# Kernel optimization log

Measured on AMD Instinct MI355X. Metric: run time of the kernel, lower is better.

The kernel has to match this reference:

```python
import jax, jax.numpy as jnp
import numpy as np

HEADS = 12
DIM_HEAD = 64
SCALE = DIM_HEAD ** -0.5

def setup_inputs() -> dict:
    key = jax.random.key(0)
    k1, k2, k3, k4 = jax.random.split(key, 4)
    dim, inner = 768, HEADS * DIM_HEAD
    x = jax.random.normal(k1, (4, 2048, dim), dtype=jnp.float32)
    w_qkv = jax.random.normal(k2, (dim, 3 * inner), dtype=jnp.float32) * (dim ** -0.5)
    w_out = jax.random.normal(k3, (inner, dim), dtype=jnp.float32) * (inner ** -0.5)
    b_out = jax.random.normal(k4, (dim,), dtype=jnp.float32) * 0.02
    return {"x": x, "w_qkv": w_qkv, "w_out": w_out, "b_out": b_out}

def reference(x, w_qkv, w_out, b_out):
    B, N, _ = x.shape
    qkv = jnp.einsum('bnd,de->bne', x, w_qkv)  # [B,N,3*inner]
    q, k, v = jnp.split(qkv, 3, axis=-1)
    # b n (h d) -> b h n d
    split_heads = lambda t: t.reshape(B, N, HEADS, DIM_HEAD).transpose(0, 2, 1, 3)
    q, k, v = split_heads(q), split_heads(k), split_heads(v)
    dots = jnp.einsum('bhnd,bhmd->bhnm', q, k) * SCALE  # [B,H,N,N]
    attn = jax.nn.softmax(dots, axis=-1)
    out = jnp.einsum('bhnm,bhmd->bhnd', attn, v)
    out = out.transpose(0, 2, 1, 3).reshape(B, N, HEADS * DIM_HEAD)  # b h n d -> b n (h d)
    return jnp.einsum('bne,ed->bnd', out, w_out) + b_out
```

## Files before the change

kernel.cpp:

```cpp
#include <hip/hip_runtime.h>
#include <stdint.h>

typedef unsigned short ushort_t;
typedef __attribute__((ext_vector_type(8))) short short8;
typedef __attribute__((ext_vector_type(4))) float f32x4;
typedef __attribute__((ext_vector_type(2))) uint32_t u32x2;

#define BATCH 4
#define SEQ 2048
#define DMODEL 768
#define NH 12
#define HD 64
#define QKV3 2304
#define NHEADS 48
#define SCALE_Q 0.18033688011112042f

__device__ __forceinline__ ushort_t f2bf(float f) {
    union { float f; uint32_t u; } v; v.f = f;
    uint32_t u = v.u;
    u += 0x7FFF + ((u >> 16) & 1);
    return (ushort_t)(u >> 16);
}

__device__ __forceinline__ uint32_t pack_bf16(float a, float b) {
#if __has_builtin(__builtin_amdgcn_cvt_pk_bf16_f32)
    typedef __attribute__((ext_vector_type(2))) __bf16 bf16x2;
    bf16x2 r = __builtin_amdgcn_cvt_pk_bf16_f32(a, b);
    return __builtin_bit_cast(uint32_t, r);
#else
    return ((uint32_t)f2bf(b) << 16) | (uint32_t)f2bf(a);
#endif
}

typedef __attribute__((address_space(1))) uint32_t as1_u32;
typedef __attribute__((address_space(3))) uint32_t as3_u32;
__device__ __forceinline__ void async16(void* lds, const void* gsrc) {
    __builtin_amdgcn_global_load_lds((as1_u32*)gsrc, (as3_u32*)lds, 16, 0, 0);
}

__device__ __forceinline__ void wait_vm_lgkm0() {
    __builtin_amdgcn_s_waitcnt(0x0070);
}

__device__ __forceinline__ void swap32(uint32_t& a, uint32_t& b) {
    asm("v_permlane32_swap_b32 %0, %1" : "+v"(a), "+v"(b));
}
__device__ __forceinline__ void swap16(uint32_t& a, uint32_t& b) {
    asm("v_permlane16_swap_b32 %0, %1" : "+v"(a), "+v"(b));
}

__global__ __launch_bounds__(256) void cvt_bf16(
    const float* __restrict__ in, ushort_t* __restrict__ out) {
    int i = blockIdx.x * 256 + threadIdx.x;
    float4 v = *(const float4*)(in + (size_t)i * 4);
    ushort4 o; o.x = f2bf(v.x); o.y = f2bf(v.y); o.z = f2bf(v.z); o.w = f2bf(v.w);
    *(ushort4*)(out + (size_t)i * 4) = o;
}

__global__ __launch_bounds__(256) void transpose_f32_bf16(
    const float* __restrict__ in, ushort_t* __restrict__ out, int R, int C) {
    __shared__ ushort_t t[64][72];
    const int tid = threadIdx.x;
    const int r0 = blockIdx.y * 64, c0 = blockIdx.x * 64;
#pragma unroll
    for (int i = 0; i < 4; i++) {
        int idx = tid + i * 256;
        int row = idx >> 4, c4 = (idx & 15) * 4;
        float4 v = *(const float4*)(in + (size_t)(r0 + row) * C + c0 + c4);
        ushort4 o; o.x = f2bf(v.x); o.y = f2bf(v.y); o.z = f2bf(v.z); o.w = f2bf(v.w);
        *(ushort4*)&t[row][c4] = o;
    }
    __syncthreads();
#pragma unroll
    for (int i = 0; i < 2; i++) {
        int idx = tid + i * 256;
        int oc = idx >> 3, g8 = (idx & 7) * 8;
        ushort_t tmp[8];
#pragma unroll
        for (int e = 0; e < 8; e++) tmp[e] = t[g8 + e][oc];
        *(short8*)(out + (size_t)(c0 + oc) * R + r0 + g8) = *(const short8*)tmp;
    }
}

__global__ __launch_bounds__(256, 2) void gemm_qkv(
    const ushort_t* __restrict__ A, const ushort_t* __restrict__ B,
    ushort_t* __restrict__ qkv, ushort_t* __restrict__ vT) {
    __shared__ ushort_t As[128 * 64];
    __shared__ ushort_t Bs[128 * 64];

    const int tid = threadIdx.x;
    const int m0 = blockIdx.y * 128, n0 = blockIdx.x * 128;
    const int lane = tid & 63, w = tid >> 6;
    const int wm = w >> 1, wn = w & 1;
    const int l16 = lane & 15, quad = lane >> 4;

    f32x4 acc[4][4];
#pragma unroll
    for (int i = 0; i < 4; i++)
#pragma unroll
        for (int j = 0; j < 4; j++) acc[i][j] = (f32x4){0.f, 0.f, 0.f, 0.f};

    int srow[4], scol[4];
#pragma unroll
    for (int j = 0; j < 4; j++) {
        int s = j * 256 + tid;
        srow[j] = s >> 3;
        scol[j] = ((s & 7) ^ (srow[j] & 7)) * 8;
    }
    const int swz0 = (quad ^ (l16 & 7)) * 8;
    const int swz1 = ((4 + quad) ^ (l16 & 7)) * 8;

    for (int kt = 0; kt < DMODEL; kt += 64) {
#pragma unroll
        for (int j = 0; j < 4; j++) {
            async16(&As[(j * 256 + w * 64) * 8],
                    A + (size_t)(m0 + srow[j]) * DMODEL + kt + scol[j]);
            async16(&Bs[(j * 256 + w * 64) * 8],
                    B + (size_t)(n0 + srow[j]) * DMODEL + kt + scol[j]);
        }
        wait_vm_lgkm0();
        __syncthreads();

        short8 a[4][2], b[4][2];
#pragma unroll
        for (int mi = 0; mi < 4; mi++) {
            int r = (wm * 64 + mi * 16 + l16) * 64;
            a[mi][0] = *(const short8*)&As[r + swz0];
            a[mi][1] = *(const short8*)&As[r + swz1];
        }
#pragma unroll
        for (int ni = 0; ni < 4; ni++) {
            int r = (wn * 64 + ni * 16 + l16) * 64;
            b[ni][0] = *(const short8*)&Bs[r + swz0];
            b[ni][1] = *(const short8*)&Bs[r + swz1];
        }
#pragma unroll
        for (int kk = 0; kk < 2; kk++)
#pragma unroll
            for (int mi = 0; mi < 4; mi++)
#pragma unroll
                for (int ni = 0; ni < 4; ni++)
                    acc[mi][ni] = __builtin_amdgcn_mfma_f32_16x16x32_bf16(
                        a[mi][kk], b[ni][kk], acc[mi][ni], 0, 0, 0);
        __syncthreads();
    }

#pragma unroll
    for (int ni = 0; ni < 4; ni++) {
        int nbase = n0 + wn * 64 + ni * 16;
        int which = nbase / DMODEL;
        int rem = nbase - which * DMODEL;
        int h = rem >> 6;
        int d = (rem & 63) + l16;
        if (which == 2) {
#pragma unroll
            for (int mi = 0; mi < 4; mi++) {
                int mg = m0 + wm * 64 + mi * 16 + quad * 4;
                int b_ = mg >> 11, ns = mg & 2047;
                u32x2 pk = {pack_bf16(acc[mi][ni][0], acc[mi][ni][1]),
                            pack_bf16(acc[mi][ni][2], acc[mi][ni][3])};
                *(u32x2*)(vT + ((size_t)(b_ * NH + h) * HD + d) * SEQ + ns) = pk;
            }
        } else {
            float scale = (which == 0) ? SCALE_Q : 1.0f;
#pragma unroll
            for (int mi = 0; mi < 4; mi++) {
#pragma unroll
                for (int r = 0; r < 4; r++) {
                    int mg = m0 + wm * 64 + mi * 16 + quad * 4 + r;
                    int b_ = mg >> 11, ns = mg & 2047;
                    size_t dst = (((size_t)(which * BATCH + b_) * NH + h) * SEQ + ns) * HD + d;
                    qkv[dst] = f2bf(acc[mi][ni][r] * scale);
                }
            }
        }
    }
}

__global__ __launch_bounds__(256, 3) void attn(
    const ushort_t* __restrict__ qkv, const ushort_t* __restrict__ vT,
    ushort_t* __restrict__ ao) {
    __shared__ ushort_t smem[16384];

    const int tid = threadIdx.x;
    const int bid = blockIdx.x;
    const int i = bid >> 3;
    const int bh = (bid & 7) + 8 * (i % 6);
    const int qt = i / 6;
    const int lane = tid & 63, w = tid >> 6;
    const int l16 = lane & 15, quad = lane >> 4;
    const int qh7 = l16 & 7;

    const ushort_t* qh = qkv + (size_t)bh * (SEQ * HD);
    const ushort_t* kh = qkv + (size_t)(NHEADS + bh) * (SEQ * HD);
    const ushort_t* vh = vT + (size_t)bh * (HD * SEQ);

    short8 aq[2][2];
#pragma unroll
    for (int mi = 0; mi < 2; mi++)
#pragma unroll
        for (int kk = 0; kk < 2; kk++) {
            int row = qt * 128 + w * 32 + mi * 16 + l16;
            aq[mi][kk] = *(const short8*)(qh + (size_t)row * HD + kk * 32 + quad * 8);
        }

    short8 ones8;
#pragma unroll
    for (int j = 0; j < 8; j++) ones8[j] = (short)0x3F80;

    f32x4 acc_l[2];
    f32x4 O[4][2];
#pragma unroll
    for (int mi = 0; mi < 2; mi++) acc_l[mi] = (f32x4){0.f, 0.f, 0.f, 0.f};
#pragma unroll
    for (int nd = 0; nd < 4; nd++)
#pragma unroll
        for (int mi = 0; mi < 2; mi++) O[nd][mi] = (f32x4){0.f, 0.f, 0.f, 0.f};

    int srow[2], scol[2];
#pragma unroll
    for (int j = 0; j < 2; j++) {
        int s = j * 256 + tid;
        srow[j] = s >> 3;
        scol[j] = ((s & 7) ^ (srow[j] & 7)) * 8;
    }
    const int swz0 = (quad ^ qh7) * 8;
    const int swz1 = ((4 + quad) ^ qh7) * 8;

#pragma unroll
    for (int j = 0; j < 2; j++) {
        async16(&smem[(j * 256 + w * 64) * 8],
                kh + (size_t)srow[j] * HD + scol[j]);
        async16(&smem[4096 + (j * 256 + w * 64) * 8],
                vh + (size_t)srow[j] * SEQ + scol[j]);
    }

    const int NT = SEQ / 64;
    for (int t = 0; t < NT; t++) {
        wait_vm_lgkm0();
        __syncthreads();
        if (t + 1 < NT) {
            int nb = ((t + 1) & 1) * 8192, j1 = (t + 1) * 64;
#pragma unroll
            for (int j = 0; j < 2; j++) {
                async16(&smem[nb + (j * 256 + w * 64) * 8],
                        kh + (size_t)(j1 + srow[j]) * HD + scol[j]);
                async16(&smem[nb + 4096 + (j * 256 + w * 64) * 8],
                        vh + (size_t)srow[j] * SEQ + j1 + scol[j]);
            }
        }
        const ushort_t* Ks = smem + (t & 1) * 8192;
        const ushort_t* Vs = Ks + 4096;

#pragma unroll
        for (int p = 0; p < 2; p++) {
            uint32_t pkv[2][2][2];
#pragma unroll
            for (int sub = 0; sub < 2; sub++) {
                const int ni = p * 2 + sub;
                int r = (ni * 16 + l16) * 64;
                short8 ak0 = *(const short8*)&Ks[r + swz0];
                short8 ak1 = *(const short8*)&Ks[r + swz1];
#pragma unroll
                for (int mi = 0; mi < 2; mi++) {
                    f32x4 s = __builtin_amdgcn_mfma_f32_16x16x32_bf16(
                        ak0, aq[mi][0], (f32x4){0.f, 0.f, 0.f, 0.f}, 0, 0, 0);
                    s = __builtin_amdgcn_mfma_f32_16x16x32_bf16(
                        ak1, aq[mi][1], s, 0, 0, 0);
                    f32x4 pr;
#pragma unroll
                    for (int rr = 0; rr < 4; rr++)
                        pr[rr] = __builtin_amdgcn_exp2f(s[rr]);
                    pkv[sub][mi][0] = pack_bf16(pr[0], pr[1]);
                    pkv[sub][mi][1] = pack_bf16(pr[2], pr[3]);
                }
            }
            short8 bp32[2];
#pragma unroll
            for (int mi = 0; mi < 2; mi++) {
                uint32_t x0 = pkv[0][mi][0], y0 = pkv[1][mi][0];
                uint32_t x1 = pkv[0][mi][1], y1 = pkv[1][mi][1];
                swap32(x0, y0); swap16(x0, y0);
                swap32(x1, y1); swap16(x1, y1);
                union { short8 s; uint32_t u[4]; } bu;
                bu.u[0] = x0; bu.u[1] = x1; bu.u[2] = y0; bu.u[3] = y1;
                bp32[mi] = bu.s;
            }
            __builtin_amdgcn_s_setprio(1);
#pragma unroll
            for (int mi = 0; mi < 2; mi++)
                acc_l[mi] = __builtin_amdgcn_mfma_f32_16x16x32_bf16(
                    ones8, bp32[mi], acc_l[mi], 0, 0, 0);
#pragma unroll
            for (int nd = 0; nd < 4; nd++) {
                int vrow = nd * 16 + l16;
                short8 av = *(const short8*)&Vs[vrow * 64 +
                                                (((p * 4 + quad) ^ qh7) * 8)];
#pragma unroll
                for (int mi = 0; mi < 2; mi++)
                    O[nd][mi] = __builtin_amdgcn_mfma_f32_16x16x32_bf16(
                        av, bp32[mi], O[nd][mi], 0, 0, 0);
            }
            __builtin_amdgcn_s_setprio(0);
        }
    }

    float inv[2];
#pragma unroll
    for (int mi = 0; mi < 2; mi++)
        inv[mi] = __builtin_amdgcn_rcpf(acc_l[mi][0]);
    wait_vm_lgkm0();
    __syncthreads();
    ushort_t* Lt = smem;
#pragma unroll
    for (int mi = 0; mi < 2; mi++)
#pragma unroll
        for (int nd = 0; nd < 4; nd++) {
            int row = w * 32 + mi * 16 + l16;
            int col = nd * 16 + quad * 4;
            uint32_t d0 = pack_bf16(O[nd][mi][0] * inv[mi], O[nd][mi][1] * inv[mi]);
            uint32_t d1 = pack_bf16(O[nd][mi][2] * inv[mi], O[nd][mi][3] * inv[mi]);
            *(u32x2*)&Lt[row * 72 + col] = (u32x2){d0, d1};
        }
    __syncthreads();

    const int b_ = bh / NH, h = bh % NH;
#pragma unroll
    for (int i2 = 0; i2 < 4; i2++) {
        int idx = tid + i2 * 256;
        int row = idx >> 3, c8 = (idx & 7) * 8;
        short8 vv = *(const short8*)&Lt[row * 72 + c8];
        *(short8*)(ao + ((size_t)(b_ * SEQ + qt * 128 + row)) * DMODEL +
                   h * HD + c8) = vv;
    }
}

__global__ __launch_bounds__(256, 2) void gemm_out(
    const ushort_t* __restrict__ A, const ushort_t* __restrict__ B,
    const float* __restrict__ bias, float* __restrict__ out) {
    __shared__ ushort_t As[128 * 64];
    __shared__ ushort_t Bs[128 * 64];

    const int tid = threadIdx.x;
    const int m0 = blockIdx.y * 128, n0 = blockIdx.x * 128;
    const int lane = tid & 63, w = tid >> 6;
    const int wm = w >> 1, wn = w & 1;
    const int l16 = lane & 15, quad = lane >> 4;

    f32x4 acc[4][4];
#pragma unroll
    for (int i = 0; i < 4; i++)
#pragma unroll
        for (int j = 0; j < 4; j++) acc[i][j] = (f32x4){0.f, 0.f, 0.f, 0.f};

    int srow[4], scol[4];
#pragma unroll
    for (int j = 0; j < 4; j++) {
        int s = j * 256 + tid;
        srow[j] = s >> 3;
        scol[j] = ((s & 7) ^ (srow[j] & 7)) * 8;
    }
    const int swz0 = (quad ^ (l16 & 7)) * 8;
    const int swz1 = ((4 + quad) ^ (l16 & 7)) * 8;

    for (int kt = 0; kt < DMODEL; kt += 64) {
#pragma unroll
        for (int j = 0; j < 4; j++) {
            async16(&As[(j * 256 + w * 64) * 8],
                    A + (size_t)(m0 + srow[j]) * DMODEL + kt + scol[j]);
            async16(&Bs[(j * 256 + w * 64) * 8],
                    B + (size_t)(n0 + srow[j]) * DMODEL + kt + scol[j]);
        }
        wait_vm_lgkm0();
        __syncthreads();

        short8 a[4][2], b[4][2];
#pragma unroll
        for (int mi = 0; mi < 4; mi++) {
            int r = (wm * 64 + mi * 16 + l16) * 64;
            a[mi][0] = *(const short8*)&As[r + swz0];
            a[mi][1] = *(const short8*)&As[r + swz1];
        }
#pragma unroll
        for (int ni = 0; ni < 4; ni++) {
            int r = (wn * 64 + ni * 16 + l16) * 64;
            b[ni][0] = *(const short8*)&Bs[r + swz0];
            b[ni][1] = *(const short8*)&Bs[r + swz1];
        }
#pragma unroll
        for (int kk = 0; kk < 2; kk++)
#pragma unroll
            for (int mi = 0; mi < 4; mi++)
#pragma unroll
                for (int ni = 0; ni < 4; ni++)
                    acc[mi][ni] = __builtin_amdgcn_mfma_f32_16x16x32_bf16(
                        a[mi][kk], b[ni][kk], acc[mi][ni], 0, 0, 0);
        __syncthreads();
    }

#pragma unroll
    for (int ni = 0; ni < 4; ni++) {
        int ng = n0 + wn * 64 + ni * 16 + l16;
        float bv = bias[ng];
#pragma unroll
        for (int mi = 0; mi < 4; mi++) {
#pragma unroll
            for (int r = 0; r < 4; r++) {
                int mg = m0 + wm * 64 + mi * 16 + quad * 4 + r;
                out[(size_t)mg * DMODEL + ng] = acc[mi][ni][r] + bv;
            }
        }
    }
}

extern "C" void kernel_launch(void* const* d_in, const int* in_sizes, int n_in,
                              void* d_out, int out_size, void* d_ws, size_t ws_size,
                              hipStream_t stream) {
    const float* x     = (const float*)d_in[0];
    const float* w_qkv = (const float*)d_in[1];
    const float* w_out = (const float*)d_in[2];
    const float* b_out = (const float*)d_in[3];
    float* out = (float*)d_out;

    ushort_t* xb  = (ushort_t*)d_ws;
    ushort_t* wqT = xb  + (size_t)8192 * 768;
    ushort_t* woT = wqT + (size_t)QKV3 * 768;
    ushort_t* qkv = woT + (size_t)768 * 768;
    ushort_t* vT  = qkv + (size_t)3 * NHEADS * SEQ * HD;
    ushort_t* ao  = vT  + (size_t)NHEADS * HD * SEQ;

    cvt_bf16<<<dim3((8192 * 768) / 4 / 256), 256, 0, stream>>>(x, xb);
    transpose_f32_bf16<<<dim3(QKV3 / 64, DMODEL / 64), 256, 0, stream>>>(
        w_qkv, wqT, DMODEL, QKV3);
    transpose_f32_bf16<<<dim3(DMODEL / 64, DMODEL / 64), 256, 0, stream>>>(
        w_out, woT, DMODEL, DMODEL);

    gemm_qkv<<<dim3(QKV3 / 128, (BATCH * SEQ) / 128), 256, 0, stream>>>(
        xb, wqT, qkv, vT);

    attn<<<dim3(NHEADS * (SEQ / 128)), 256, 0, stream>>>(qkv, vT, ao);

    gemm_out<<<dim3(DMODEL / 128, (BATCH * SEQ) / 128), 256, 0, stream>>>(
        ao, woT, b_out, out);
}
```

Measured before the change: 211.1 us.

## Load V tiles directly into registers instead of staging through LDS

V fragments are now loaded from global memory straight into registers, double-buffered across a two-tile unrolled loop, instead of being copied asynchronously into shared memory and read back. This halves the LDS footprint and removes the LDS reads for V. Each wave now issues its own redundant global loads of V, since all four waves read the same tile, and register pressure rises by 16 short8 values, which may hurt occupancy under launch_bounds 3.

```diff
diff --git a/kernel.cpp b/kernel.cpp
--- a/kernel.cpp
+++ b/kernel.cpp
@@ -180,7 +180,7 @@
 __global__ __launch_bounds__(256, 3) void attn(
     const ushort_t* __restrict__ qkv, const ushort_t* __restrict__ vT,
     ushort_t* __restrict__ ao) {
-    __shared__ ushort_t smem[16384];
+    __shared__ ushort_t smem[9216];
 
     const int tid = threadIdx.x;
     const int bid = blockIdx.x;
@@ -194,6 +194,7 @@
     const ushort_t* qh = qkv + (size_t)bh * (SEQ * HD);
     const ushort_t* kh = qkv + (size_t)(NHEADS + bh) * (SEQ * HD);
     const ushort_t* vh = vT + (size_t)bh * (HD * SEQ);
+    const ushort_t* vbase = vh + (size_t)l16 * SEQ + quad * 8;
 
     short8 aq[2][2];
 #pragma unroll
@@ -227,30 +228,35 @@
     const int swz0 = (quad ^ qh7) * 8;
     const int swz1 = ((4 + quad) ^ qh7) * 8;
 
-#pragma unroll
-    for (int j = 0; j < 2; j++) {
+    auto vload = [&](short8 (&vd)[8], int t) {
+#pragma unroll
+        for (int p = 0; p < 2; p++)
+#pragma unroll
+            for (int nd = 0; nd < 4; nd++)
+                vd[p * 4 + nd] = *(const short8*)(
+                    vbase + (size_t)nd * 16 * SEQ + t * 64 + p * 32);
+    };
+
+#pragma unroll
+    for (int j = 0; j < 2; j++)
         async16(&smem[(j * 256 + w * 64) * 8],
                 kh + (size_t)srow[j] * HD + scol[j]);
-        async16(&smem[4096 + (j * 256 + w * 64) * 8],
-                vh + (size_t)srow[j] * SEQ + scol[j]);
-    }
+    short8 vA[8], vB[8];
+    vload(vA, 0);
 
     const int NT = SEQ / 64;
-    for (int t = 0; t < NT; t++) {
+    auto tile_body = [&](short8 (&vcur)[8], short8 (&vnxt)[8], int t) {
         wait_vm_lgkm0();
         __syncthreads();
         if (t + 1 < NT) {
-            int nb = ((t + 1) & 1) * 8192, j1 = (t + 1) * 64;
-#pragma unroll
-            for (int j = 0; j < 2; j++) {
+            int nb = ((t + 1) & 1) * 4096, j1 = (t + 1) * 64;
+#pragma unroll
+            for (int j = 0; j < 2; j++)
                 async16(&smem[nb + (j * 256 + w * 64) * 8],
                         kh + (size_t)(j1 + srow[j]) * HD + scol[j]);
-                async16(&smem[nb + 4096 + (j * 256 + w * 64) * 8],
-                        vh + (size_t)srow[j] * SEQ + j1 + scol[j]);
-            }
-        }
-        const ushort_t* Ks = smem + (t & 1) * 8192;
-        const ushort_t* Vs = Ks + 4096;
+            vload(vnxt, t + 1);
+        }
+        const ushort_t* Ks = smem + (t & 1) * 4096;
 
 #pragma unroll
         for (int p = 0; p < 2; p++) {
@@ -293,16 +299,18 @@
                     ones8, bp32[mi], acc_l[mi], 0, 0, 0);
 #pragma unroll
             for (int nd = 0; nd < 4; nd++) {
-                int vrow = nd * 16 + l16;
-                short8 av = *(const short8*)&Vs[vrow * 64 +
-                                                (((p * 4 + quad) ^ qh7) * 8)];
 #pragma unroll
                 for (int mi = 0; mi < 2; mi++)
                     O[nd][mi] = __builtin_amdgcn_mfma_f32_16x16x32_bf16(
-                        av, bp32[mi], O[nd][mi], 0, 0, 0);
+                        vcur[p * 4 + nd], bp32[mi], O[nd][mi], 0, 0, 0);
             }
             __builtin_amdgcn_s_setprio(0);
         }
+    };
+
+    for (int t = 0; t < NT; t += 2) {
+        tile_body(vA, vB, t);
+        tile_body(vB, vA, t + 1);
     }
 
     float inv[2];
```

New measurement: 269.4 us. +27.6%, slower.
